# Optimization experiments

Measured on AMD Instinct MI355X. Metric: run time of the kernel, lower is better.

The kernel has to match this reference:

```python
import jax, jax.numpy as jnp
import numpy as np
from jax import lax

T, B, C = 50, 50, 4096
PADLEN = 49
ORDER = 2
BANDS = [(0.05, 0.15), (0.2, 0.4)]


def _butter_bandpass_sos(n, w1, w2):
    """Butterworth bandpass design (scipy.signal.iirfilter(..., ftype='butter', output='sos') equivalent)."""
    fs = 2.0
    warped = 2.0 * fs * np.tan(np.pi * np.array([w1, w2]) / fs)  # pre-warped analog freqs
    bw = warped[1] - warped[0]
    wo = np.sqrt(warped[0] * warped[1])
    k = np.arange(1, n + 1)
    p = -np.exp(1j * np.pi * (2 * k - 1) / (2 * n))  # analog LP prototype poles
    # lp2bp: n poles -> 2n poles, n zeros at origin, gain *= bw**n
    p_lp = p * bw / 2.0
    disc = np.sqrt(p_lp ** 2 - wo ** 2 + 0j)
    p_bp = np.concatenate([p_lp + disc, p_lp - disc])
    # bilinear transform (fs=2): zeros at origin -> +1; n zeros at infinity -> -1
    fs2 = 2.0 * fs
    p_d = (fs2 + p_bp) / (fs2 - p_bp)
    gain = (bw ** n) * (fs2 ** n) / np.real(np.prod(fs2 - p_bp))
    # pair conjugate poles into biquads; numerator (z-1)(z+1) = [1, 0, -1]
    pos = p_d[np.imag(p_d) > 0]
    assert len(pos) == n, 'expected complex-conjugate pole pairs'
    sos = []
    for i, pp in enumerate(pos):
        a = np.array([1.0, -2.0 * np.real(pp), np.abs(pp) ** 2])
        b = np.array([1.0, 0.0, -1.0])
        if i == 0:
            b = b * gain
        sos.append(np.concatenate([b, a]))
    return np.array(sos)  # [n_sections, 6]


def _sosfilt_zi(sos):
    """scipy.signal.sosfilt_zi: steady-state per-section initial conditions (DF2T)."""
    n_sections = sos.shape[0]
    zi = np.zeros((n_sections, 2))
    scale = 1.0
    for s in range(n_sections):
        b, a = sos[s, :3], sos[s, 3:]
        B0 = b[1] - a[1] * b[0]
        B1 = b[2] - a[2] * b[0]
        det = 1.0 + a[1] + a[2]
        zi[s, 0] = scale * (B0 + B1) / det
        zi[s, 1] = scale * ((1.0 + a[1]) * B1 - a[2] * B0) / det
        scale *= b.sum() / a.sum()
    return zi


def _sosfilt(sos, x, zi):
    """Cascaded biquads, direct form II transposed, scan over time axis 0.
    x: [T, B, C]; zi: list of (z0, z1) each [B, C]."""
    y = x
    for s in range(sos.shape[0]):
        b0, b1, b2 = (float(sos[s, 0]), float(sos[s, 1]), float(sos[s, 2]))
        a1, a2 = float(sos[s, 4]), float(sos[s, 5])
        def step(carry, xt, b0=b0, b1=b1, b2=b2, a1=a1, a2=a2):
            z0, z1 = carry
            yt = b0 * xt + z0
            return (b1 * xt + z1 - a1 * yt, b2 * xt - a2 * yt), yt
        _, y = lax.scan(step, (zi[s][0], zi[s][1]), y)
    return y


def _odd_ext(x, n):
    left = 2.0 * x[0] - x[n:0:-1]
    right = 2.0 * x[-1] - x[-2:-n - 2:-1]
    return jnp.concatenate([left, x, right], axis=0)


def _sosfiltfilt(sos, x, padlen):
    zi = _sosfilt_zi(sos)  # [S, 2] numpy
    ext = _odd_ext(x, padlen)  # [T + 2*padlen, B, C]
    x0 = ext[0]
    zi_f = [(float(zi[s, 0]) * x0, float(zi[s, 1]) * x0) for s in range(sos.shape[0])]
    y = _sosfilt(sos, ext, zi_f)
    y = y[::-1]
    y0 = y[0]
    zi_b = [(float(zi[s, 0]) * y0, float(zi[s, 1]) * y0) for s in range(sos.shape[0])]
    y = _sosfilt(sos, y, zi_b)
    y = y[::-1]
    return y[padlen:-padlen]


def _tensor_zscore(x):
    # Faithful to the original expand([50,-1,-1]).permute(1,0,2) quirk:
    # mean/std over axis 0 give [B, C]; the permute aligns them with the TIME axis,
    # i.e. out[t, b, c] = (x[t, b, c] - m[t, c]) / s[t, c]  (valid since T == B == 50).
    m = x.mean(axis=0)
    s = x.std(axis=0, ddof=1)  # torch.std default is unbiased
    return (x - m[:, None, :]) / s[:, None, :]


def setup_inputs() -> dict:
    key = jax.random.key(0)
    sample = jax.random.normal(key, (T, B, C), dtype=jnp.float32)
    return {"sample": sample}


def reference(sample):
    outs = []
    for (w1, w2) in BANDS:
        sos = _butter_bandpass_sos(ORDER, w1, w2)
        y = _sosfiltfilt(sos, sample, PADLEN)
        y = y - y.mean(axis=0)  # bandpass branch: mean-center
        y = _tensor_zscore(y)   # normalize=True
        outs.append(y)
    return jnp.stack(outs)  # [n_bands, T, B, C]
```

## Files before the change

kernel.cpp:

```cpp
#include <hip/hip_runtime.h>
#include <hip/hip_bf16.h>
#include <cmath>
#include <complex>

constexpr int TT  = 50;
constexpr int NB  = 50;
constexpr int NC  = 4096;
constexpr int NCH = NB * NC;
constexpr int PAD = 49;
constexpr int EXT = TT + 2 * PAD;
constexpr int CT  = 16;

struct Coefs {
    double b0[2][2], b1[2][2], b2[2][2], a1[2][2], a2[2][2];
    double zi0[2][2], zi1[2][2];
};

__global__ void __launch_bounds__(64) build_M(float* __restrict__ Mt, Coefs cf) {
    __shared__ double e[EXT][TT];
    const int band = blockIdx.x;
    const int j = threadIdx.x;
    if (j >= TT) return;

#pragma unroll
    for (int i = 0; i < PAD; ++i)
        e[i][j] = 2.0 * (j == 0 ? 1.0 : 0.0) - ((PAD - i) == j ? 1.0 : 0.0);
#pragma unroll
    for (int t = 0; t < TT; ++t) e[PAD + t][j] = (t == j) ? 1.0 : 0.0;
#pragma unroll
    for (int i = 0; i < PAD; ++i)
        e[PAD + TT + i][j] = 2.0 * (j == TT - 1 ? 1.0 : 0.0) - ((TT - 2 - i) == j ? 1.0 : 0.0);

    const double x0 = e[0][j];
#pragma unroll
    for (int s = 0; s < 2; ++s) {
        const double b0 = cf.b0[band][s], b1 = cf.b1[band][s], b2 = cf.b2[band][s];
        const double a1 = cf.a1[band][s], a2 = cf.a2[band][s];
        double z0 = cf.zi0[band][s] * x0, z1 = cf.zi1[band][s] * x0;
#pragma unroll
        for (int i = 0; i < EXT; ++i) {
            const double xt = e[i][j];
            const double yt = b0 * xt + z0;
            z0 = b1 * xt + z1 - a1 * yt;
            z1 = b2 * xt - a2 * yt;
            e[i][j] = yt;
        }
    }
    const double y0 = e[EXT - 1][j];
#pragma unroll
    for (int s = 0; s < 2; ++s) {
        const double b0 = cf.b0[band][s], b1 = cf.b1[band][s], b2 = cf.b2[band][s];
        const double a1 = cf.a1[band][s], a2 = cf.a2[band][s];
        double z0 = cf.zi0[band][s] * y0, z1 = cf.zi1[band][s] * y0;
#pragma unroll
        for (int m = 0; m < EXT; ++m) {
            const int i = EXT - 1 - m;
            const double xt = e[i][j];
            const double yt = b0 * xt + z0;
            z0 = b1 * xt + z1 - a1 * yt;
            z1 = b2 * xt - a2 * yt;
            e[i][j] = yt;
        }
    }
    double mean = 0.0;
#pragma unroll
    for (int t = 0; t < TT; ++t) mean += e[PAD + t][j];
    mean *= (1.0 / TT);
#pragma unroll
    for (int t = 0; t < TT; ++t)
        Mt[(band * TT + j) * TT + t] = (float)(e[PAD + t][j] - mean);
}

__global__ void __launch_bounds__(CT * NB, 1)
filt_main(const float* __restrict__ x, const float* __restrict__ Mt,
          float* __restrict__ out) {
    const int tx = threadIdx.x;
    const int b  = threadIdx.y;
    const int c  = blockIdx.x * CT + tx;
    const int i  = b * NC + c;

    __shared__ float sm_mu[NB][CT];
    __shared__ float sm_inv[NB][CT];

    for (int band = 0; band < 2; ++band) {
        float f[TT];
#pragma unroll
        for (int t = 0; t < TT; ++t) f[t] = 0.f;

        for (int k = 0; k < TT; ++k) {
            const float xk = x[(size_t)k * NCH + i];
            const float* __restrict__ r = Mt + (band * TT + k) * TT;
#pragma unroll
            for (int t = 0; t < TT; ++t) f[t] = fmaf(r[t], xk, f[t]);
        }

        float mu = 0.f;
#pragma unroll
        for (int t = 0; t < TT; ++t) mu += f[t];
        mu *= (1.0f / TT);
        float ss = 0.f;
#pragma unroll
        for (int t = 0; t < TT; ++t) {
            const float h = f[t] - mu;
            ss = fmaf(h, h, ss);
        }
        const float inv = 1.0f / sqrtf(ss * (1.0f / (TT - 1)));
        sm_mu[b][tx] = mu;
        sm_inv[b][tx] = inv;
        __syncthreads();

#pragma unroll
        for (int t = 0; t < TT; ++t) {
            const float v = (f[t] - sm_mu[t][tx]) * sm_inv[t][tx];
            out[(size_t)(band * TT + t) * NCH + i] = v;
        }
        __syncthreads();
    }
}

static Coefs make_coefs() {
    Coefs cf;
    const double bands[2][2] = {{0.05, 0.15}, {0.2, 0.4}};
    const int n = 2;
    for (int bd = 0; bd < 2; ++bd) {
        const double fs = 2.0;
        const double w1 = bands[bd][0], w2 = bands[bd][1];
        const double warped0 = 2.0 * fs * std::tan(M_PI * w1 / fs);
        const double warped1 = 2.0 * fs * std::tan(M_PI * w2 / fs);
        const double bw = warped1 - warped0;
        const double wo = std::sqrt(warped0 * warped1);
        std::complex<double> p_bp[4];
        for (int k = 1; k <= n; ++k) {
            std::complex<double> p = -std::exp(std::complex<double>(0.0, M_PI * (2 * k - 1) / (2.0 * n)));
            std::complex<double> plp = p * (bw / 2.0);
            std::complex<double> disc = std::sqrt(plp * plp - std::complex<double>(wo * wo, 0.0));
            p_bp[k - 1] = plp + disc;
            p_bp[n + k - 1] = plp - disc;
        }
        const double fs2 = 2.0 * fs;
        std::complex<double> prod(1.0, 0.0);
        for (int i = 0; i < 2 * n; ++i) prod *= (fs2 - p_bp[i]);
        const double gain = std::pow(bw, n) * std::pow(fs2, n) / prod.real();
        std::complex<double> p_d[4];
        for (int i = 0; i < 2 * n; ++i) p_d[i] = (fs2 + p_bp[i]) / (fs2 - p_bp[i]);
        double sos[2][6];
        int cnt = 0;
        for (int i = 0; i < 2 * n; ++i) {
            if (p_d[i].imag() > 0) {
                const double g = (cnt == 0) ? gain : 1.0;
                sos[cnt][0] = g;
                sos[cnt][1] = 0.0;
                sos[cnt][2] = -g;
                sos[cnt][3] = 1.0;
                sos[cnt][4] = -2.0 * p_d[i].real();
                sos[cnt][5] = std::norm(p_d[i]);
                ++cnt;
            }
        }
        double scale = 1.0;
        for (int s = 0; s < 2; ++s) {
            const double b0 = sos[s][0], b1 = sos[s][1], b2 = sos[s][2];
            const double a1 = sos[s][4], a2 = sos[s][5];
            const double B0 = b1 - a1 * b0, B1 = b2 - a2 * b0;
            const double det = 1.0 + a1 + a2;
            cf.b0[bd][s] = b0; cf.b1[bd][s] = b1; cf.b2[bd][s] = b2;
            cf.a1[bd][s] = a1; cf.a2[bd][s] = a2;
            cf.zi0[bd][s] = scale * (B0 + B1) / det;
            cf.zi1[bd][s] = scale * ((1.0 + a1) * B1 - a2 * B0) / det;
            scale *= (b0 + b1 + b2) / (1.0 + a1 + a2);
        }
    }
    return cf;
}

extern "C" void kernel_launch(void* const* d_in, const int* in_sizes, int n_in,
                              void* d_out, int out_size, void* d_ws, size_t ws_size,
                              hipStream_t stream) {
    const float* x = (const float*)d_in[0];
    float* out = (float*)d_out;
    float* Mt = (float*)d_ws;

    const Coefs cf = make_coefs();
    build_M<<<dim3(2), dim3(64), 0, stream>>>(Mt, cf);
    filt_main<<<dim3(NC / CT), dim3(CT, NB), 0, stream>>>(x, Mt, out);
}
```

Measured before the change: 152.4 us.

## Fuse both bands into one pass over input and move build_M state to registers

```diff
diff --git a/kernel.cpp b/kernel.cpp
--- a/kernel.cpp
+++ b/kernel.cpp
@@ -16,22 +16,22 @@
     double zi0[2][2], zi1[2][2];
 };
 
-__global__ void __launch_bounds__(64) build_M(float* __restrict__ Mt, Coefs cf) {
-    __shared__ double e[EXT][TT];
+__global__ void __launch_bounds__(64, 1) build_M(float* __restrict__ Mt, Coefs cf) {
     const int band = blockIdx.x;
     const int j = threadIdx.x;
     if (j >= TT) return;
 
+    double e[EXT];
 #pragma unroll
     for (int i = 0; i < PAD; ++i)
-        e[i][j] = 2.0 * (j == 0 ? 1.0 : 0.0) - ((PAD - i) == j ? 1.0 : 0.0);
+        e[i] = 2.0 * (j == 0 ? 1.0 : 0.0) - ((PAD - i) == j ? 1.0 : 0.0);
 #pragma unroll
-    for (int t = 0; t < TT; ++t) e[PAD + t][j] = (t == j) ? 1.0 : 0.0;
+    for (int t = 0; t < TT; ++t) e[PAD + t] = (t == j) ? 1.0 : 0.0;
 #pragma unroll
     for (int i = 0; i < PAD; ++i)
-        e[PAD + TT + i][j] = 2.0 * (j == TT - 1 ? 1.0 : 0.0) - ((TT - 2 - i) == j ? 1.0 : 0.0);
+        e[PAD + TT + i] = 2.0 * (j == TT - 1 ? 1.0 : 0.0) - ((TT - 2 - i) == j ? 1.0 : 0.0);
 
-    const double x0 = e[0][j];
+    const double x0 = e[0];
 #pragma unroll
     for (int s = 0; s < 2; ++s) {
         const double b0 = cf.b0[band][s], b1 = cf.b1[band][s], b2 = cf.b2[band][s];
@@ -39,14 +39,14 @@
         double z0 = cf.zi0[band][s] * x0, z1 = cf.zi1[band][s] * x0;
 #pragma unroll
         for (int i = 0; i < EXT; ++i) {
-            const double xt = e[i][j];
+            const double xt = e[i];
             const double yt = b0 * xt + z0;
             z0 = b1 * xt + z1 - a1 * yt;
             z1 = b2 * xt - a2 * yt;
-            e[i][j] = yt;
+            e[i] = yt;
         }
     }
-    const double y0 = e[EXT - 1][j];
+    const double y0 = e[EXT - 1];
 #pragma unroll
     for (int s = 0; s < 2; ++s) {
         const double b0 = cf.b0[band][s], b1 = cf.b1[band][s], b2 = cf.b2[band][s];
@@ -55,23 +55,23 @@
 #pragma unroll
         for (int m = 0; m < EXT; ++m) {
             const int i = EXT - 1 - m;
-            const double xt = e[i][j];
+            const double xt = e[i];
             const double yt = b0 * xt + z0;
             z0 = b1 * xt + z1 - a1 * yt;
             z1 = b2 * xt - a2 * yt;
-            e[i][j] = yt;
+            e[i] = yt;
         }
     }
     double mean = 0.0;
 #pragma unroll
-    for (int t = 0; t < TT; ++t) mean += e[PAD + t][j];
+    for (int t = 0; t < TT; ++t) mean += e[PAD + t];
     mean *= (1.0 / TT);
 #pragma unroll
     for (int t = 0; t < TT; ++t)
-        Mt[(band * TT + j) * TT + t] = (float)(e[PAD + t][j] - mean);
+        Mt[(band * TT + j) * TT + t] = (float)(e[PAD + t] - mean);
 }
 
-__global__ void __launch_bounds__(CT * NB, 1)
+__global__ void __launch_bounds__(CT * NB, 4)
 filt_main(const float* __restrict__ x, const float* __restrict__ Mt,
           float* __restrict__ out) {
     const int tx = threadIdx.x;
@@ -79,42 +79,46 @@
     const int c  = blockIdx.x * CT + tx;
     const int i  = b * NC + c;
 
-    __shared__ float sm_mu[NB][CT];
-    __shared__ float sm_inv[NB][CT];
+    __shared__ float smu0[NB][CT], sinv0[NB][CT];
+    __shared__ float smu1[NB][CT], sinv1[NB][CT];
 
-    for (int band = 0; band < 2; ++band) {
-        float f[TT];
+    float f0[TT], f1[TT];
 #pragma unroll
-        for (int t = 0; t < TT; ++t) f[t] = 0.f;
+    for (int t = 0; t < TT; ++t) { f0[t] = 0.f; f1[t] = 0.f; }
 
-        for (int k = 0; k < TT; ++k) {
-            const float xk = x[(size_t)k * NCH + i];
-            const float* __restrict__ r = Mt + (band * TT + k) * TT;
+    const float* __restrict__ M0 = Mt;
+    const float* __restrict__ M1 = Mt + TT * TT;
+
 #pragma unroll
-            for (int t = 0; t < TT; ++t) f[t] = fmaf(r[t], xk, f[t]);
-        }
-
-        float mu = 0.f;
-#pragma unroll
-        for (int t = 0; t < TT; ++t) mu += f[t];
-        mu *= (1.0f / TT);
-        float ss = 0.f;
+    for (int k = 0; k < TT; ++k) {
+        const float xk = x[(size_t)k * NCH + i];
 #pragma unroll
         for (int t = 0; t < TT; ++t) {
-            const float h = f[t] - mu;
-            ss = fmaf(h, h, ss);
+            f0[t] = fmaf(M0[k * TT + t], xk, f0[t]);
+            f1[t] = fmaf(M1[k * TT + t], xk, f1[t]);
         }
-        const float inv = 1.0f / sqrtf(ss * (1.0f / (TT - 1)));
-        sm_mu[b][tx] = mu;
-        sm_inv[b][tx] = inv;
-        __syncthreads();
+    }
+
+    float mu0 = 0.f, mu1 = 0.f;
+#pragma unroll
+    for (int t = 0; t < TT; ++t) { mu0 += f0[t]; mu1 += f1[t]; }
+    mu0 *= (1.0f / TT); mu1 *= (1.0f / TT);
+    float ss0 = 0.f, ss1 = 0.f;
+#pragma unroll
+    for (int t = 0; t < TT; ++t) {
+        const float h0 = f0[t] - mu0; ss0 = fmaf(h0, h0, ss0);
+        const float h1 = f1[t] - mu1; ss1 = fmaf(h1, h1, ss1);
+    }
+    smu0[b][tx] = mu0; sinv0[b][tx] = 1.0f / sqrtf(ss0 * (1.0f / (TT - 1)));
+    smu1[b][tx] = mu1; sinv1[b][tx] = 1.0f / sqrtf(ss1 * (1.0f / (TT - 1)));
+    __syncthreads();
 
 #pragma unroll
-        for (int t = 0; t < TT; ++t) {
-            const float v = (f[t] - sm_mu[t][tx]) * sm_inv[t][tx];
-            out[(size_t)(band * TT + t) * NCH + i] = v;
-        }
-        __syncthreads();
+    for (int t = 0; t < TT; ++t) {
+        out[(size_t)t * NCH + i] =
+            (f0[t] - smu0[t][tx]) * sinv0[t][tx];
+        out[(size_t)(TT + t) * NCH + i] =
+            (f1[t] - smu1[t][tx]) * sinv1[t][tx];
     }
 }
 
```

Measured after the change: 168.4 us. +10.5%, slower.

## Fuse biquad cascade in build_M and raise filt_main occupancy bound

Applied to the files above, without the earlier changes.

```diff
diff --git a/kernel.cpp b/kernel.cpp
--- a/kernel.cpp
+++ b/kernel.cpp
@@ -16,62 +16,65 @@
     double zi0[2][2], zi1[2][2];
 };
 
-__global__ void __launch_bounds__(64) build_M(float* __restrict__ Mt, Coefs cf) {
-    __shared__ double e[EXT][TT];
+__global__ void __launch_bounds__(64, 1) build_M(float* __restrict__ Mt, Coefs cf) {
+    __shared__ float ylds[EXT][TT];
     const int band = blockIdx.x;
     const int j = threadIdx.x;
     if (j >= TT) return;
 
+    const double b00 = cf.b0[band][0], b10 = cf.b1[band][0], b20 = cf.b2[band][0];
+    const double a10 = cf.a1[band][0], a20 = cf.a2[band][0];
+    const double b01 = cf.b0[band][1], b11 = cf.b1[band][1], b21 = cf.b2[band][1];
+    const double a11 = cf.a1[band][1], a21 = cf.a2[band][1];
+
+    const double x0 = 2.0 * (j == 0 ? 1.0 : 0.0) - (j == PAD ? 1.0 : 0.0);
+
+    double s00 = cf.zi0[band][0] * x0, s01 = cf.zi1[band][0] * x0;
+    double s10 = cf.zi0[band][1] * x0, s11 = cf.zi1[band][1] * x0;
+    double ylast = 0.0;
 #pragma unroll
-    for (int i = 0; i < PAD; ++i)
-        e[i][j] = 2.0 * (j == 0 ? 1.0 : 0.0) - ((PAD - i) == j ? 1.0 : 0.0);
+    for (int i = 0; i < EXT; ++i) {
+        double xt;
+        if (i < PAD)            xt = 2.0 * (j == 0 ? 1.0 : 0.0) - (j == PAD - i ? 1.0 : 0.0);
+        else if (i < PAD + TT)  xt = (j == i - PAD) ? 1.0 : 0.0;
+        else                    xt = 2.0 * (j == TT - 1 ? 1.0 : 0.0)
+                                     - (j == 2 * TT - 2 - (i - PAD) ? 1.0 : 0.0);
+        const double y0 = b00 * xt + s00;
+        s00 = b10 * xt + s01 - a10 * y0;
+        s01 = b20 * xt - a20 * y0;
+        const double y1 = b01 * y0 + s10;
+        s10 = b11 * y0 + s11 - a11 * y1;
+        s11 = b21 * y0 - a21 * y1;
+        ylds[i][j] = (float)y1;
+        if (i == EXT - 1) ylast = y1;
+    }
+
+    s00 = cf.zi0[band][0] * ylast; s01 = cf.zi1[band][0] * ylast;
+    s10 = cf.zi0[band][1] * ylast; s11 = cf.zi1[band][1] * ylast;
+    float o[TT];
 #pragma unroll
-    for (int t = 0; t < TT; ++t) e[PAD + t][j] = (t == j) ? 1.0 : 0.0;
+    for (int m = 0; m < EXT; ++m) {
+        const int i = EXT - 1 - m;
+        const double xt = (double)ylds[i][j];
+        const double y0 = b00 * xt + s00;
+        s00 = b10 * xt + s01 - a10 * y0;
+        s01 = b20 * xt - a20 * y0;
+        const double y1 = b01 * y0 + s10;
+        s10 = b11 * y0 + s11 - a11 * y1;
+        s11 = b21 * y0 - a21 * y1;
+        if (i >= PAD && i < PAD + TT) o[i - PAD] = (float)y1;
+    }
+
+    float mean = 0.f;
 #pragma unroll
-    for (int i = 0; i < PAD; ++i)
-        e[PAD + TT + i][j] = 2.0 * (j == TT - 1 ? 1.0 : 0.0) - ((TT - 2 - i) == j ? 1.0 : 0.0);
-
-    const double x0 = e[0][j];
-#pragma unroll
-    for (int s = 0; s < 2; ++s) {
-        const double b0 = cf.b0[band][s], b1 = cf.b1[band][s], b2 = cf.b2[band][s];
-        const double a1 = cf.a1[band][s], a2 = cf.a2[band][s];
-        double z0 = cf.zi0[band][s] * x0, z1 = cf.zi1[band][s] * x0;
-#pragma unroll
-        for (int i = 0; i < EXT; ++i) {
-            const double xt = e[i][j];
-            const double yt = b0 * xt + z0;
-            z0 = b1 * xt + z1 - a1 * yt;
-            z1 = b2 * xt - a2 * yt;
-            e[i][j] = yt;
-        }
-    }
-    const double y0 = e[EXT - 1][j];
-#pragma unroll
-    for (int s = 0; s < 2; ++s) {
-        const double b0 = cf.b0[band][s], b1 = cf.b1[band][s], b2 = cf.b2[band][s];
-        const double a1 = cf.a1[band][s], a2 = cf.a2[band][s];
-        double z0 = cf.zi0[band][s] * y0, z1 = cf.zi1[band][s] * y0;
-#pragma unroll
-        for (int m = 0; m < EXT; ++m) {
-            const int i = EXT - 1 - m;
-            const double xt = e[i][j];
-            const double yt = b0 * xt + z0;
-            z0 = b1 * xt + z1 - a1 * yt;
-            z1 = b2 * xt - a2 * yt;
-            e[i][j] = yt;
-        }
-    }
-    double mean = 0.0;
-#pragma unroll
-    for (int t = 0; t < TT; ++t) mean += e[PAD + t][j];
-    mean *= (1.0 / TT);
+    for (int t = 0; t < TT; ++t) mean += o[t];
+    mean *= (1.0f / TT);
 #pragma unroll
     for (int t = 0; t < TT; ++t)
-        Mt[(band * TT + j) * TT + t] = (float)(e[PAD + t][j] - mean);
+        Mt[(band * TT + j) * TT + t] = o[t] - mean;
 }
 
-__global__ void __launch_bounds__(CT * NB, 1)
+__global__ void __launch_bounds__(CT * NB, 3)
 filt_main(const float* __restrict__ x, const float* __restrict__ Mt,
           float* __restrict__ out) {
     const int tx = threadIdx.x;
@@ -79,19 +82,20 @@
     const int c  = blockIdx.x * CT + tx;
     const int i  = b * NC + c;
 
-    __shared__ float sm_mu[NB][CT];
-    __shared__ float sm_inv[NB][CT];
+    __shared__ float smu[NB][CT], sinv[NB][CT];
 
+#pragma unroll 1
     for (int band = 0; band < 2; ++band) {
+        const float* __restrict__ Mb = Mt + band * TT * TT;
         float f[TT];
 #pragma unroll
         for (int t = 0; t < TT; ++t) f[t] = 0.f;
 
+#pragma unroll
         for (int k = 0; k < TT; ++k) {
             const float xk = x[(size_t)k * NCH + i];
-            const float* __restrict__ r = Mt + (band * TT + k) * TT;
 #pragma unroll
-            for (int t = 0; t < TT; ++t) f[t] = fmaf(r[t], xk, f[t]);
+            for (int t = 0; t < TT; ++t) f[t] = fmaf(Mb[k * TT + t], xk, f[t]);
         }
 
         float mu = 0.f;
@@ -104,16 +108,14 @@
             const float h = f[t] - mu;
             ss = fmaf(h, h, ss);
         }
-        const float inv = 1.0f / sqrtf(ss * (1.0f / (TT - 1)));
-        sm_mu[b][tx] = mu;
-        sm_inv[b][tx] = inv;
+        smu[b][tx] = mu;
+        sinv[b][tx] = 1.0f / sqrtf(ss * (1.0f / (TT - 1)));
         __syncthreads();
 
 #pragma unroll
-        for (int t = 0; t < TT; ++t) {
-            const float v = (f[t] - sm_mu[t][tx]) * sm_inv[t][tx];
-            out[(size_t)(band * TT + t) * NCH + i] = v;
-        }
+        for (int t = 0; t < TT; ++t)
+            out[(size_t)(band * TT + t) * NCH + i] =
+                (f[t] - smu[t][tx]) * sinv[t][tx];
         __syncthreads();
     }
 }
```

Result: slower. 159.8 us (+4.8%).
